# Performance work log

Measured on AMD Instinct MI355X. Metric: run time of the kernel, lower is better.

Reference implementation:

```python
import jax, jax.numpy as jnp
import numpy as np

NUM_NODES = 100000
PROP_STEP = 8


def _spmm(vals, rows, cols, x):
    # sparse [N,N] @ dense [N,F]: gather source rows, scale, scatter-add to dest
    gathered = x[cols] * vals[:, None]  # [E, F]
    return jax.ops.segment_sum(gathered, rows, num_segments=NUM_NODES)


def setup_inputs() -> dict:
    key = jax.random.key(0)
    k1, k2, k3, k4, k5 = jax.random.split(key, 5)
    N, E, C = NUM_NODES, 3200000, 128
    x = jax.random.normal(k1, (N, C), dtype=jnp.float32)
    # xavier_uniform for weight [c_in, c_out]
    limit = float(np.sqrt(6.0 / (C + C)))
    weight = jax.random.uniform(k2, (C, C), dtype=jnp.float32, minval=-limit, maxval=limit)
    lap_vals = jax.random.uniform(k3, (E,), dtype=jnp.float32)
    lap_rows = jax.random.randint(k4, (E,), 0, N, dtype=jnp.int64)
    lap_cols = jax.random.randint(k5, (E,), 0, N, dtype=jnp.int64)
    return {"x": x, "weight": weight, "lap_vals": lap_vals,
            "lap_rows": lap_rows, "lap_cols": lap_cols}


def reference(x, weight, lap_vals, lap_rows, lap_cols):
    # filter_type='low', dropout inactive (eval / p=0)
    identity = x
    out = x @ weight  # [N, c_out]
    for _ in range(PROP_STEP):
        out = _spmm(lap_vals, lap_rows, lap_cols, out)
    return identity + out
```

## Files before the change

### kernel.cpp

```cpp
#include <hip/hip_runtime.h>
#include <hip/hip_bf16.h>
#include <hip/hip_fp16.h>
#include <stdint.h>

#define CCH 128
#define FINAL_SCALE 268435456.0f
#define RND 2048
#define BUKSH 9
#define BUKROWS 512
#define MAXBUK 256
#define COLMASK 0x1FFFF
#define SLABCAP 17408


__global__ __launch_bounds__(256) void part_kernel(const int* __restrict__ rows,
                                                   const int* __restrict__ cols,
                                                   const float* __restrict__ vals,
                                                   int* __restrict__ gcur,
                                                   unsigned int* __restrict__ rec_rc,
                                                   float* __restrict__ rec_v,
                                                   int E, int nbuk) {
    __shared__ int hist[MAXBUK];
    __shared__ int offs[MAXBUK];
    __shared__ int cur[MAXBUK];
    __shared__ int gbase[MAXBUK];
    __shared__ unsigned int stage_rc[RND];
    __shared__ float stage_v[RND];
    __shared__ unsigned char stage_b[RND];

    int base = blockIdx.x * RND;
    int cnt = E - base;
    if (cnt > RND) cnt = RND;
    if (cnt <= 0) return;

    for (int i = threadIdx.x; i < nbuk; i += 256) hist[i] = 0;
    __syncthreads();

    int myr[RND / 256], myc[RND / 256];
    float myv[RND / 256];
#pragma unroll
    for (int k = 0; k < RND / 256; ++k) {
        int li = k * 256 + threadIdx.x;
        bool ok = li < cnt;
        int gi = base + li;
        myr[k] = ok ? rows[gi] : -1;
        myc[k] = ok ? cols[gi] : 0;
        myv[k] = ok ? vals[gi] : 0.f;
        if (ok) atomicAdd(&hist[myr[k] >> BUKSH], 1);
    }
    __syncthreads();

    if (threadIdx.x == 0) {
        int run = 0;
        for (int b = 0; b < nbuk; ++b) {
            offs[b] = run;
            cur[b] = run;
            run += hist[b];
        }
    }
    __syncthreads();
    if (threadIdx.x < nbuk) gbase[threadIdx.x] = atomicAdd(&gcur[threadIdx.x], hist[threadIdx.x]);
    __syncthreads();

#pragma unroll
    for (int k = 0; k < RND / 256; ++k) {
        if (myr[k] >= 0) {
            int b = myr[k] >> BUKSH;
            int p = atomicAdd(&cur[b], 1);
            stage_rc[p] = ((unsigned int)(myr[k] & (BUKROWS - 1)) << 17) | (unsigned int)myc[k];
            stage_v[p] = myv[k];
            stage_b[p] = (unsigned char)b;
        }
    }
    __syncthreads();

    for (int i = threadIdx.x; i < cnt; i += 256) {
        int b = stage_b[i];
        size_t d = (size_t)b * SLABCAP + gbase[b] + (i - offs[b]);
        rec_rc[d] = stage_rc[i];
        rec_v[d] = stage_v[i];
    }
}

__global__ __launch_bounds__(MAXBUK) void slab_scan_kernel(const int* __restrict__ gcur,
                                                           int* __restrict__ bukbase,
                                                           int* __restrict__ row_ptr,
                                                           int nbuk, int n, int E) {
    __shared__ int tile[MAXBUK];
    int t = threadIdx.x;
    tile[t] = (t < nbuk) ? gcur[t] : 0;
    __syncthreads();
    for (int off = 1; off < MAXBUK; off <<= 1) {
        int add = (t >= off) ? tile[t - off] : 0;
        __syncthreads();
        tile[t] += add;
        __syncthreads();
    }
    int excl = (t == 0) ? 0 : tile[t - 1];
    if (t < nbuk) bukbase[t] = excl;
    if (t == nbuk - 1) bukbase[nbuk] = tile[t];
    if (t == 0) row_ptr[n] = E;
}

__global__ __launch_bounds__(512) void csrfill2_kernel(const unsigned int* __restrict__ rec_rc,
                                                       const float* __restrict__ rec_v,
                                                       const int* __restrict__ bukbase,
                                                       int* __restrict__ row_ptr,
                                                       int2* __restrict__ edges,
                                                       int n) {
    __shared__ int lcnt[BUKROWS];
    __shared__ int lscan[BUKROWS];
    __shared__ int lfill[BUKROWS];
    int bucket = blockIdx.x;
    int r0 = bucket << BUKSH;
    if (r0 >= n) return;
    int t = threadIdx.x;
    size_t sbase = (size_t)bucket * SLABCAP;
    int gb = bukbase[bucket];
    int cnt = bukbase[bucket + 1] - gb;

    lcnt[t] = 0;
    __syncthreads();

    for (int i = t; i < cnt; i += 512)
        atomicAdd(&lcnt[rec_rc[sbase + i] >> 17], 1);
    __syncthreads();

    int v = lcnt[t];
    lscan[t] = v;
    __syncthreads();
    for (int off = 1; off < 512; off <<= 1) {
        int add = (t >= off) ? lscan[t - off] : 0;
        __syncthreads();
        lscan[t] += add;
        __syncthreads();
    }
    int excl = lscan[t] - v;

    int r = r0 + t;
    if (r < n) row_ptr[r] = gb + excl;

    lfill[t] = 0;
    lcnt[t] = gb + excl;
    __syncthreads();

    int i = t;
    for (; i + 512 < cnt; i += 1024) {
        unsigned int wa = rec_rc[sbase + i];
        unsigned int wb = rec_rc[sbase + i + 512];
        float va = rec_v[sbase + i];
        float vb = rec_v[sbase + i + 512];
        int ra = wa >> 17, rb = wb >> 17;
        int pa = lcnt[ra] + atomicAdd(&lfill[ra], 1);
        int pb = lcnt[rb] + atomicAdd(&lfill[rb], 1);
        edges[pa] = make_int2((int)(wa & COLMASK), __float_as_int(va));
        edges[pb] = make_int2((int)(wb & COLMASK), __float_as_int(vb));
    }
    if (i < cnt) {
        unsigned int wa = rec_rc[sbase + i];
        float va = rec_v[sbase + i];
        int ra = wa >> 17;
        int pa = lcnt[ra] + atomicAdd(&lfill[ra], 1);
        edges[pa] = make_int2((int)(wa & COLMASK), __float_as_int(va));
    }
}


typedef _Float16 f16x8 __attribute__((ext_vector_type(8)));
typedef float f32x4 __attribute__((ext_vector_type(4)));
typedef short s4_t __attribute__((ext_vector_type(4)));

#define WT_LD 136
#define TR_LD (CCH + 8)

__global__ __launch_bounds__(256) void gemm_kernel(const float* __restrict__ x,
                                                   const float* __restrict__ w,
                                                   __half* __restrict__ out, int n) {
    __shared__ _Float16 wt[CCH * WT_LD];
    __shared__ __half tr[4][16][TR_LD];
    int tid = threadIdx.x;
#pragma unroll
    for (int i = 0; i < 16; ++i) {
        int idx = i * 256 + tid;
        float4 v = ((const float4*)w)[idx];
        int k = idx >> 5;
        int c0 = (idx & 31) << 2;
        wt[(c0 + 0) * WT_LD + k] = (_Float16)v.x;
        wt[(c0 + 1) * WT_LD + k] = (_Float16)v.y;
        wt[(c0 + 2) * WT_LD + k] = (_Float16)v.z;
        wt[(c0 + 3) * WT_LD + k] = (_Float16)v.w;
    }
    __syncthreads();

    int lane = tid & 63;
    int wave = tid >> 6;
    int lr = lane & 15;
    int lg = lane >> 4;
    int rbase = blockIdx.x * 64 + wave * 16;

    f16x8 a[4];
    int arow = rbase + lr;
    if (arow < n) {
        const float* xp = x + (size_t)arow * CCH;
#pragma unroll
        for (int kt = 0; kt < 4; ++kt) {
            float4 f0 = *(const float4*)(xp + kt * 32 + lg * 4);
            float4 f1 = *(const float4*)(xp + kt * 32 + 16 + lg * 4);
            f16x8 a8;
            a8[0] = (_Float16)f0.x; a8[1] = (_Float16)f0.y;
            a8[2] = (_Float16)f0.z; a8[3] = (_Float16)f0.w;
            a8[4] = (_Float16)f1.x; a8[5] = (_Float16)f1.y;
            a8[6] = (_Float16)f1.z; a8[7] = (_Float16)f1.w;
            a[kt] = a8;
        }
    } else {
        f16x8 z = {};
#pragma unroll
        for (int kt = 0; kt < 4; ++kt) a[kt] = z;
    }

    f32x4 acc[8];
#pragma unroll
    for (int ct = 0; ct < 8; ++ct) acc[ct] = (f32x4){0.f, 0.f, 0.f, 0.f};

#pragma unroll
    for (int ct = 0; ct < 8; ++ct) {
        const _Float16* bp = &wt[(ct * 16 + lr) * WT_LD];
#pragma unroll
        for (int kt = 0; kt < 4; ++kt) {
            union { s4_t s[2]; f16x8 h; } u;
            u.s[0] = *(const s4_t*)(bp + kt * 32 + lg * 4);
            u.s[1] = *(const s4_t*)(bp + kt * 32 + 16 + lg * 4);
            acc[ct] = __builtin_amdgcn_mfma_f32_16x16x32_f16(a[kt], u.h, acc[ct], 0, 0, 0);
        }
    }

#pragma unroll
    for (int ct = 0; ct < 8; ++ct)
#pragma unroll
        for (int reg = 0; reg < 4; ++reg)
            tr[wave][lg * 4 + reg][ct * 16 + lr] = __float2half(acc[ct][reg]);

    int row = lane >> 2;
    int seg = lane & 3;
    int orow = rbase + row;
    if (orow < n) {
#pragma unroll
        for (int it = 0; it < 4; ++it) {
            float4 v = *(const float4*)&tr[wave][row][it * 32 + seg * 8];
            *(float4*)(out + (size_t)orow * CCH + it * 32 + seg * 8) = v;
        }
    }
}


template <int FINAL>
__global__ __launch_bounds__(256) void spmm_kernel(const int* __restrict__ row_ptr,
                                                   const int2* __restrict__ edges,
                                                   const __half* __restrict__ src,
                                                   __half* __restrict__ dsth,
                                                   float* __restrict__ dstf,
                                                   const float* __restrict__ identity,
                                                   int n) {
    int lane = threadIdx.x & 63;
    int row = (blockIdx.x * blockDim.x + threadIdx.x) >> 6;
    if (row >= n) return;
    int g = lane >> 4;
    int gl = lane & 15;

    int s = row_ptr[row];
    int e = row_ptr[row + 1];

    float acc[8] = {};

    for (int base = s; base < e; base += 16) {
        int2 ed[4];
        float4 gv[4];
#pragma unroll
        for (int t = 0; t < 4; ++t) {
            int idx = base + g * 4 + t;
            bool ok = idx < e;
            ed[t] = edges[ok ? idx : s];
            if (!ok) ed[t].y = 0;
        }
#pragma unroll
        for (int t = 0; t < 4; ++t)
            gv[t] = *(const float4*)(src + (size_t)ed[t].x * CCH + gl * 8);
#pragma unroll
        for (int t = 0; t < 4; ++t) {
            float v = __int_as_float(ed[t].y);
            const __half* h = (const __half*)&gv[t];
#pragma unroll
            for (int j = 0; j < 8; ++j)
                acc[j] += v * __half2float(h[j]);
        }
    }

#pragma unroll
    for (int j = 0; j < 8; ++j) {
        acc[j] += __shfl_xor(acc[j], 16, 64);
        acc[j] += __shfl_xor(acc[j], 32, 64);
    }

    if (FINAL) {
        if (g == 0) {
            const float* iv = identity + (size_t)row * CCH + gl * 8;
            float4 o;
            o.x = iv[0] + acc[0] * FINAL_SCALE;
            o.y = iv[1] + acc[1] * FINAL_SCALE;
            o.z = iv[2] + acc[2] * FINAL_SCALE;
            o.w = iv[3] + acc[3] * FINAL_SCALE;
            *(float4*)(dstf + (size_t)row * CCH + gl * 8) = o;
        } else if (g == 1) {
            const float* iv = identity + (size_t)row * CCH + gl * 8 + 4;
            float4 o;
            o.x = iv[0] + acc[4] * FINAL_SCALE;
            o.y = iv[1] + acc[5] * FINAL_SCALE;
            o.z = iv[2] + acc[6] * FINAL_SCALE;
            o.w = iv[3] + acc[7] * FINAL_SCALE;
            *(float4*)(dstf + (size_t)row * CCH + gl * 8 + 4) = o;
        }
    } else {
        if (g == 0) {
            __half2 h[4];
            h[0] = __float22half2_rn(make_float2(acc[0] * 0.0625f, acc[1] * 0.0625f));
            h[1] = __float22half2_rn(make_float2(acc[2] * 0.0625f, acc[3] * 0.0625f));
            h[2] = __float22half2_rn(make_float2(acc[4] * 0.0625f, acc[5] * 0.0625f));
            h[3] = __float22half2_rn(make_float2(acc[6] * 0.0625f, acc[7] * 0.0625f));
            *(float4*)(dsth + (size_t)row * CCH + gl * 8) = *(float4*)h;
        }
    }
}


static inline size_t align256(size_t x) { return (x + 255) & ~(size_t)255; }

extern "C" void kernel_launch(void* const* d_in, const int* in_sizes, int n_in,
                              void* d_out, int out_size, void* d_ws, size_t ws_size,
                              hipStream_t stream) {
    const float* x = (const float*)d_in[0];
    const float* w = (const float*)d_in[1];
    const float* lap_vals = (const float*)d_in[2];
    const int* lap_rows = (const int*)d_in[3];
    const int* lap_cols = (const int*)d_in[4];

    const int N = in_sizes[0] / CCH;
    const int E = in_sizes[2];
    const int NBUK = (N + BUKROWS - 1) >> BUKSH;

    char* ws = (char*)d_ws;
    size_t off = 0;
    __half* bufA = (__half*)(ws + off); off = align256(off + (size_t)N * CCH * sizeof(__half));
    __half* bufB = (__half*)(ws + off); off = align256(off + (size_t)N * CCH * sizeof(__half));
    int2* edges = (int2*)(ws + off);    off = align256(off + (size_t)E * sizeof(int2) + 16);
    int* row_ptr = (int*)(ws + off);    off = align256(off + (size_t)(N + 1) * sizeof(int));
    int* bukbase = (int*)(ws + off);    off = align256(off + (size_t)(MAXBUK + 1) * sizeof(int));
    int* gcur = (int*)(ws + off);       off = align256(off + (size_t)MAXBUK * sizeof(int));
    (void)ws_size;
    unsigned int* rec_rc = (unsigned int*)bufA;
    float* rec_v = (float*)((char*)bufA + (size_t)NBUK * SLABCAP * sizeof(unsigned int));

    float* out = (float*)d_out;

    hipMemsetAsync(gcur, 0, (size_t)MAXBUK * sizeof(int), stream);

    part_kernel<<<(E + RND - 1) / RND, 256, 0, stream>>>(lap_rows, lap_cols, lap_vals,
                                                         gcur, rec_rc, rec_v, E, NBUK);
    slab_scan_kernel<<<1, MAXBUK, 0, stream>>>(gcur, bukbase, row_ptr, NBUK, N, E);
    csrfill2_kernel<<<NBUK, 512, 0, stream>>>(rec_rc, rec_v, bukbase, row_ptr, edges, N);

    gemm_kernel<<<(N + 63) / 64, 256, 0, stream>>>(x, w, bufA, N);

    int spmm_blocks = (N + 3) / 4;
    const __half* src = bufA;
    __half* dst = bufB;
    for (int step = 1; step <= 7; ++step) {
        spmm_kernel<0><<<spmm_blocks, 256, 0, stream>>>(row_ptr, edges, src, dst, nullptr, nullptr, N);
        __half* t = (__half*)src;
        src = dst;
        dst = t;
    }
    spmm_kernel<1><<<spmm_blocks, 256, 0, stream>>>(row_ptr, edges, src, nullptr, out, x, N);
}
```

Before: 1.062 ms.

## Pack edge column and fp16 value into one 32-bit word; widen GEMM blocks

Edge values are converted to fp16 and packed with the 17-bit column index into a single 32-bit word. This halves edge storage and the edge-stream bandwidth in each of the eight SpMM passes, and also shrinks the partition staging buffers. Separately, the GEMM kernel now uses 512-thread blocks covering 128 rows and reuses the weight shared memory for the output transpose. The cost is reduced precision on edge values, since fp16 keeps only about 11 significant bits.

```diff
diff --git a/kernel.cpp b/kernel.cpp
--- a/kernel.cpp
+++ b/kernel.cpp
@@ -12,20 +12,33 @@
 #define COLMASK 0x1FFFF
 #define SLABCAP 17408
 
+__device__ __forceinline__ float unpack_val(unsigned int w) {
+    unsigned short b = (unsigned short)(w >> 17);
+    __half h;
+    __builtin_memcpy(&h, &b, 2);
+    return __half2float(h);
+}
+__device__ __forceinline__ unsigned short pack_val(float v) {
+    __half h = __float2half_rn(v);
+    unsigned short b;
+    __builtin_memcpy(&b, &h, 2);
+    return b;
+}
+
 
 __global__ __launch_bounds__(256) void part_kernel(const int* __restrict__ rows,
                                                    const int* __restrict__ cols,
                                                    const float* __restrict__ vals,
                                                    int* __restrict__ gcur,
                                                    unsigned int* __restrict__ rec_rc,
-                                                   float* __restrict__ rec_v,
+                                                   unsigned short* __restrict__ rec_hv,
                                                    int E, int nbuk) {
     __shared__ int hist[MAXBUK];
     __shared__ int offs[MAXBUK];
     __shared__ int cur[MAXBUK];
     __shared__ int gbase[MAXBUK];
     __shared__ unsigned int stage_rc[RND];
-    __shared__ float stage_v[RND];
+    __shared__ unsigned short stage_hv[RND];
     __shared__ unsigned char stage_b[RND];
 
     int base = blockIdx.x * RND;
@@ -68,7 +81,7 @@
             int b = myr[k] >> BUKSH;
             int p = atomicAdd(&cur[b], 1);
             stage_rc[p] = ((unsigned int)(myr[k] & (BUKROWS - 1)) << 17) | (unsigned int)myc[k];
-            stage_v[p] = myv[k];
+            stage_hv[p] = pack_val(myv[k]);
             stage_b[p] = (unsigned char)b;
         }
     }
@@ -78,7 +91,7 @@
         int b = stage_b[i];
         size_t d = (size_t)b * SLABCAP + gbase[b] + (i - offs[b]);
         rec_rc[d] = stage_rc[i];
-        rec_v[d] = stage_v[i];
+        rec_hv[d] = stage_hv[i];
     }
 }
 
@@ -103,10 +116,10 @@
 }
 
 __global__ __launch_bounds__(512) void csrfill2_kernel(const unsigned int* __restrict__ rec_rc,
-                                                       const float* __restrict__ rec_v,
+                                                       const unsigned short* __restrict__ rec_hv,
                                                        const int* __restrict__ bukbase,
                                                        int* __restrict__ row_ptr,
-                                                       int2* __restrict__ edges,
+                                                       unsigned int* __restrict__ edges,
                                                        int n) {
     __shared__ int lcnt[BUKROWS];
     __shared__ int lscan[BUKROWS];
@@ -148,20 +161,20 @@
     for (; i + 512 < cnt; i += 1024) {
         unsigned int wa = rec_rc[sbase + i];
         unsigned int wb = rec_rc[sbase + i + 512];
-        float va = rec_v[sbase + i];
-        float vb = rec_v[sbase + i + 512];
+        unsigned int va = rec_hv[sbase + i];
+        unsigned int vb = rec_hv[sbase + i + 512];
         int ra = wa >> 17, rb = wb >> 17;
         int pa = lcnt[ra] + atomicAdd(&lfill[ra], 1);
         int pb = lcnt[rb] + atomicAdd(&lfill[rb], 1);
-        edges[pa] = make_int2((int)(wa & COLMASK), __float_as_int(va));
-        edges[pb] = make_int2((int)(wb & COLMASK), __float_as_int(vb));
+        edges[pa] = (va << 17) | (wa & COLMASK);
+        edges[pb] = (vb << 17) | (wb & COLMASK);
     }
     if (i < cnt) {
         unsigned int wa = rec_rc[sbase + i];
-        float va = rec_v[sbase + i];
+        unsigned int va = rec_hv[sbase + i];
         int ra = wa >> 17;
         int pa = lcnt[ra] + atomicAdd(&lfill[ra], 1);
-        edges[pa] = make_int2((int)(wa & COLMASK), __float_as_int(va));
+        edges[pa] = (va << 17) | (wa & COLMASK);
     }
 }
 
@@ -171,17 +184,17 @@
 typedef short s4_t __attribute__((ext_vector_type(4)));
 
 #define WT_LD 136
-#define TR_LD (CCH + 8)
-
-__global__ __launch_bounds__(256) void gemm_kernel(const float* __restrict__ x,
+#define TR_LD 136
+
+__global__ __launch_bounds__(512) void gemm_kernel(const float* __restrict__ x,
                                                    const float* __restrict__ w,
                                                    __half* __restrict__ out, int n) {
-    __shared__ _Float16 wt[CCH * WT_LD];
-    __shared__ __half tr[4][16][TR_LD];
+    __shared__ _Float16 smem[CCH * WT_LD];
+    _Float16* wt = smem;
     int tid = threadIdx.x;
 #pragma unroll
-    for (int i = 0; i < 16; ++i) {
-        int idx = i * 256 + tid;
+    for (int i = 0; i < 8; ++i) {
+        int idx = i * 512 + tid;
         float4 v = ((const float4*)w)[idx];
         int k = idx >> 5;
         int c0 = (idx & 31) << 2;
@@ -196,7 +209,7 @@
     int wave = tid >> 6;
     int lr = lane & 15;
     int lg = lane >> 4;
-    int rbase = blockIdx.x * 64 + wave * 16;
+    int rbase = blockIdx.x * 128 + wave * 16;
 
     f16x8 a[4];
     int arow = rbase + lr;
@@ -235,11 +248,14 @@
         }
     }
 
+    __syncthreads();
+    __half* tr = (__half*)smem + (size_t)wave * 16 * TR_LD;
+
 #pragma unroll
     for (int ct = 0; ct < 8; ++ct)
 #pragma unroll
         for (int reg = 0; reg < 4; ++reg)
-            tr[wave][lg * 4 + reg][ct * 16 + lr] = __float2half(acc[ct][reg]);
+            tr[(lg * 4 + reg) * TR_LD + ct * 16 + lr] = __float2half(acc[ct][reg]);
 
     int row = lane >> 2;
     int seg = lane & 3;
@@ -247,7 +263,7 @@
     if (orow < n) {
 #pragma unroll
         for (int it = 0; it < 4; ++it) {
-            float4 v = *(const float4*)&tr[wave][row][it * 32 + seg * 8];
+            float4 v = *(const float4*)&tr[row * TR_LD + it * 32 + seg * 8];
             *(float4*)(out + (size_t)orow * CCH + it * 32 + seg * 8) = v;
         }
     }
@@ -256,7 +272,7 @@
 
 template <int FINAL>
 __global__ __launch_bounds__(256) void spmm_kernel(const int* __restrict__ row_ptr,
-                                                   const int2* __restrict__ edges,
+                                                   const unsigned int* __restrict__ edges,
                                                    const __half* __restrict__ src,
                                                    __half* __restrict__ dsth,
                                                    float* __restrict__ dstf,
@@ -274,21 +290,21 @@
     float acc[8] = {};
 
     for (int base = s; base < e; base += 16) {
-        int2 ed[4];
+        unsigned int ed[4];
         float4 gv[4];
 #pragma unroll
         for (int t = 0; t < 4; ++t) {
             int idx = base + g * 4 + t;
             bool ok = idx < e;
             ed[t] = edges[ok ? idx : s];
-            if (!ok) ed[t].y = 0;
+            if (!ok) ed[t] = 0;
         }
 #pragma unroll
         for (int t = 0; t < 4; ++t)
-            gv[t] = *(const float4*)(src + (size_t)ed[t].x * CCH + gl * 8);
+            gv[t] = *(const float4*)(src + (size_t)(ed[t] & COLMASK) * CCH + gl * 8);
 #pragma unroll
         for (int t = 0; t < 4; ++t) {
-            float v = __int_as_float(ed[t].y);
+            float v = unpack_val(ed[t]);
             const __half* h = (const __half*)&gv[t];
 #pragma unroll
             for (int j = 0; j < 8; ++j)
@@ -352,24 +368,24 @@
     size_t off = 0;
     __half* bufA = (__half*)(ws + off); off = align256(off + (size_t)N * CCH * sizeof(__half));
     __half* bufB = (__half*)(ws + off); off = align256(off + (size_t)N * CCH * sizeof(__half));
-    int2* edges = (int2*)(ws + off);    off = align256(off + (size_t)E * sizeof(int2) + 16);
+    unsigned int* edges = (unsigned int*)(ws + off); off = align256(off + (size_t)E * sizeof(unsigned int) + 16);
     int* row_ptr = (int*)(ws + off);    off = align256(off + (size_t)(N + 1) * sizeof(int));
     int* bukbase = (int*)(ws + off);    off = align256(off + (size_t)(MAXBUK + 1) * sizeof(int));
     int* gcur = (int*)(ws + off);       off = align256(off + (size_t)MAXBUK * sizeof(int));
     (void)ws_size;
     unsigned int* rec_rc = (unsigned int*)bufA;
-    float* rec_v = (float*)((char*)bufA + (size_t)NBUK * SLABCAP * sizeof(unsigned int));
+    unsigned short* rec_hv = (unsigned short*)((char*)bufA + (size_t)NBUK * SLABCAP * sizeof(unsigned int));
 
     float* out = (float*)d_out;
 
     hipMemsetAsync(gcur, 0, (size_t)MAXBUK * sizeof(int), stream);
 
     part_kernel<<<(E + RND - 1) / RND, 256, 0, stream>>>(lap_rows, lap_cols, lap_vals,
-                                                         gcur, rec_rc, rec_v, E, NBUK);
+                                                         gcur, rec_rc, rec_hv, E, NBUK);
     slab_scan_kernel<<<1, MAXBUK, 0, stream>>>(gcur, bukbase, row_ptr, NBUK, N, E);
-    csrfill2_kernel<<<NBUK, 512, 0, stream>>>(rec_rc, rec_v, bukbase, row_ptr, edges, N);
-
-    gemm_kernel<<<(N + 63) / 64, 256, 0, stream>>>(x, w, bufA, N);
+    csrfill2_kernel<<<NBUK, 512, 0, stream>>>(rec_rc, rec_hv, bukbase, row_ptr, edges, N);
+
+    gemm_kernel<<<(N + 127) / 128, 512, 0, stream>>>(x, w, bufA, N);
 
     int spmm_blocks = (N + 3) / 4;
     const __half* src = bufA;
```

Result: faster. 1.035 ms (-2.5%).
